# Performance work log

Measured on AMD Instinct MI355X. Metric: run time of the kernel, lower is better.

Reference implementation:

```python
import jax, jax.numpy as jnp
import numpy as np

N_NODES = 50000
N_EDGES = 800000
IN_DIM = 128
HID = 64
OUT = 64
HEADS = 4
NEG_SLOPE = 0.2  # DGL GATConv default leaky_relu negative slope


def gat_conv(x, src, dst, W, attn_l, attn_r, bias, n_heads, d_out, n_nodes):
    """DGL-style GATConv: x [N, F_in] -> [N, H, D]."""
    feat = (x @ W).reshape(n_nodes, n_heads, d_out)            # [N,H,D]
    el = jnp.sum(feat * attn_l, axis=-1)                        # [N,H]
    er = jnp.sum(feat * attn_r, axis=-1)                        # [N,H]
    e = jax.nn.leaky_relu(el[src] + er[dst], NEG_SLOPE)         # [E,H]
    # edge softmax over incoming edges of each dst node
    emax = jax.ops.segment_max(e, dst, num_segments=n_nodes)    # [N,H]
    emax = jnp.where(jnp.isfinite(emax), emax, 0.0)
    emax = jax.lax.stop_gradient(emax)
    a = jnp.exp(e - emax[dst])                                  # [E,H]
    denom = jax.ops.segment_sum(a, dst, num_segments=n_nodes)   # [N,H]
    alpha = a / jnp.maximum(denom[dst], 1e-9)                   # [E,H]
    msg = feat[src] * alpha[:, :, None]                         # [E,H,D]
    out = jax.ops.segment_sum(msg, dst, num_segments=n_nodes)   # [N,H,D]
    return out + bias.reshape(1, n_heads, d_out)


def setup_inputs() -> dict:
    key = jax.random.key(0)
    ks = jax.random.split(key, 12)
    features = jax.random.normal(ks[0], (N_NODES, IN_DIM), jnp.float32)
    src = jax.random.randint(ks[1], (N_EDGES,), 0, N_NODES)
    dst = jax.random.randint(ks[2], (N_EDGES,), 0, N_NODES)
    s1 = 1.0 / np.sqrt(IN_DIM)
    s2 = 1.0 / np.sqrt(HID * HEADS)
    return {
        "features": features,
        "src": src,
        "dst": dst,
        "W1": jax.random.normal(ks[3], (IN_DIM, HEADS * HID), jnp.float32) * s1,
        "al1": jax.random.normal(ks[4], (HEADS, HID), jnp.float32) * s1,
        "ar1": jax.random.normal(ks[5], (HEADS, HID), jnp.float32) * s1,
        "b1": jnp.zeros((HEADS * HID,), jnp.float32),
        "W2": jax.random.normal(ks[6], (HEADS * HID, HEADS * OUT), jnp.float32) * s2,
        "al2": jax.random.normal(ks[7], (HEADS, OUT), jnp.float32) * s2,
        "ar2": jax.random.normal(ks[8], (HEADS, OUT), jnp.float32) * s2,
        "b2": jnp.zeros((HEADS * OUT,), jnp.float32),
    }


def reference(features, src, dst, W1, al1, ar1, b1, W2, al2, ar2, b2):
    h = gat_conv(features, src, dst, W1, al1, ar1, b1, HEADS, HID, N_NODES)
    h = jax.nn.elu(h)                        # layer1 activation=F.elu
    h = h.reshape(N_NODES, HEADS * HID)      # .flatten(1)
    # dropout(0.2) is identity in eval mode
    h = gat_conv(h, src, dst, W2, al2, ar2, b2, HEADS, OUT, N_NODES)
    return h.mean(axis=1)                    # mean over heads -> [N, OUT]
```

## Files before the change

### kernel.cpp

```cpp
#include <hip/hip_runtime.h>
#include <hip/hip_bf16.h>
#include <math.h>

#define N_NODES 50000
#define N_EDGES 800000
#define IN_DIM 128
#define NEG_SLOPE 0.2f

typedef __attribute__((ext_vector_type(8))) short s16x8;
typedef __attribute__((ext_vector_type(4))) float f32x4;

__device__ inline unsigned short f2bf(float v) {
    unsigned u = __float_as_uint(v);
    unsigned r = (u + 0x7fffu + ((u >> 16) & 1u)) >> 16;
    return (unsigned short)r;
}
__device__ inline float bf2f(unsigned short b) {
    return __uint_as_float(((unsigned)b) << 16);
}
__device__ inline float lrelu(float v) {
    return v >= 0.f ? v : NEG_SLOPE * v;
}


__global__ void zero_int(int* __restrict__ p, int n) {
    int i = blockIdx.x * blockDim.x + threadIdx.x;
    if (i < n) p[i] = 0;
}

__global__ void hist_kernel(const int* __restrict__ dst, int* __restrict__ cnt) {
    int e = blockIdx.x * blockDim.x + threadIdx.x;
    if (e < N_EDGES) atomicAdd(&cnt[dst[e]], 1);
}

__global__ __launch_bounds__(1024) void scan_kernel(const int* __restrict__ cnt,
                                                    int* __restrict__ off, int n) {
    __shared__ int wsum[16];
    __shared__ int carry_s;
    int tid = threadIdx.x, wid = tid >> 6, lane = tid & 63;
    if (tid == 0) carry_s = 0;
    __syncthreads();
    for (int base = 0; base < n; base += 1024) {
        int i = base + tid;
        int v = (i < n) ? cnt[i] : 0;
        int x = v;
#pragma unroll
        for (int s = 1; s < 64; s <<= 1) {
            int t = __shfl_up(x, s, 64);
            if (lane >= s) x += t;
        }
        if (lane == 63) wsum[wid] = x;
        __syncthreads();
        if (wid == 0 && lane < 16) {
            int w = wsum[lane];
#pragma unroll
            for (int s = 1; s < 16; s <<= 1) {
                int t = __shfl_up(w, s, 64);
                if (lane >= s) w += t;
            }
            wsum[lane] = w;
        }
        __syncthreads();
        int woff = (wid > 0) ? wsum[wid - 1] : 0;
        int incl = carry_s + woff + x;
        if (i < n) off[i] = incl - v;
        __syncthreads();
        if (tid == 1023) carry_s = incl;
        __syncthreads();
    }
    if (threadIdx.x == 0) off[n] = carry_s;
}

__global__ void copy_int(const int* __restrict__ a, int* __restrict__ b, int n) {
    int i = blockIdx.x * blockDim.x + threadIdx.x;
    if (i < n) b[i] = a[i];
}

__global__ void scatter_kernel(const int* __restrict__ src, const int* __restrict__ dst,
                               int* __restrict__ cur, int* __restrict__ csr_src) {
    int e = blockIdx.x * blockDim.x + threadIdx.x;
    if (e < N_EDGES) {
        int d = dst[e];
        int pos = atomicAdd(&cur[d], 1);
        csr_src[pos] = src[e];
    }
}


__global__ void split_feat(const float* __restrict__ in, unsigned short* __restrict__ hi,
                           unsigned short* __restrict__ lo, int n4) {
    int i = blockIdx.x * blockDim.x + threadIdx.x;
    if (i < n4) {
        float4 v = *reinterpret_cast<const float4*>(&in[i * 4]);
        ushort4 h, l;
        h.x = f2bf(v.x); l.x = f2bf(v.x - bf2f(h.x));
        h.y = f2bf(v.y); l.y = f2bf(v.y - bf2f(h.y));
        h.z = f2bf(v.z); l.z = f2bf(v.z - bf2f(h.z));
        h.w = f2bf(v.w); l.w = f2bf(v.w - bf2f(h.w));
        *reinterpret_cast<ushort4*>(&hi[i * 4]) = h;
        *reinterpret_cast<ushort4*>(&lo[i * 4]) = l;
    }
}

template <int K>
__global__ void split_wt(const float* __restrict__ W, unsigned short* __restrict__ Bth,
                         unsigned short* __restrict__ Btl) {
    int k = blockIdx.x;
    int c = threadIdx.x;
    float v = W[(size_t)k * 256 + c];
    unsigned short h = f2bf(v);
    Bth[(size_t)c * K + k] = h;
    Btl[(size_t)c * K + k] = f2bf(v - bf2f(h));
}


#define GLDS(gsrc, loff)                                                        \
    __builtin_amdgcn_global_load_lds(                                           \
        (const __attribute__((address_space(1))) unsigned int*)(gsrc),          \
        (__attribute__((address_space(3))) unsigned int*)(lds + (loff)),        \
        16, 0, 0)

template <int K>
__global__ __launch_bounds__(256, 2) void mfma_gemm(const unsigned short* __restrict__ Ahi,
                                                    const unsigned short* __restrict__ Alo,
                                                    const unsigned short* __restrict__ Bth,
                                                    const unsigned short* __restrict__ Btl,
                                                    const float* __restrict__ attl,
                                                    const float* __restrict__ attr,
                                                    unsigned short* __restrict__ Chi,
                                                    float* __restrict__ el,
                                                    float* __restrict__ er,
                                                    int M) {
    __shared__ __align__(16) char lds[81920];
    int tid = threadIdx.x;
    int h = tid >> 6;
    int lane = tid & 63;
    int rr = lane & 15;
    int g = lane >> 4;
    int row0 = blockIdx.x * 64;

    int arow = row0 + (tid & 63);
    if (arow >= M) arow = M - 1;
    int akc = tid >> 6;
    const unsigned short* asrc_h = Ahi + (size_t)arow * K + akc * 8;
    const unsigned short* asrc_l = Alo + (size_t)arow * K + akc * 8;
    const unsigned short* bsrc_h = Bth + (size_t)tid * K;
    const unsigned short* bsrc_l = Btl + (size_t)tid * K;

    f32x4 acc[4][4] = {};

    {
        GLDS(asrc_h, tid * 16);
        GLDS(asrc_l, 4096 + tid * 16);
#pragma unroll
        for (int j = 0; j < 4; j++) {
            GLDS(bsrc_h + j * 8, 8192 + j * 4096 + tid * 16);
            GLDS(bsrc_l + j * 8, 24576 + j * 4096 + tid * 16);
        }
    }

    int cur = 0;
    for (int kb = 0; kb < K; kb += 32) {
        __syncthreads();
        if (kb + 32 < K) {
            int nb = (cur ^ 1) * 40960;
            GLDS(asrc_h + kb + 32, nb + tid * 16);
            GLDS(asrc_l + kb + 32, nb + 4096 + tid * 16);
#pragma unroll
            for (int j = 0; j < 4; j++) {
                GLDS(bsrc_h + kb + 32 + j * 8, nb + 8192 + j * 4096 + tid * 16);
                GLDS(bsrc_l + kb + 32 + j * 8, nb + 24576 + j * 4096 + tid * 16);
            }
        }
        const char* lb = lds + cur * 40960;
        s16x8 ah[4], al[4], bh[4], bl[4];
#pragma unroll
        for (int mi = 0; mi < 4; mi++) {
            int off = g * 1024 + (mi * 16 + rr) * 16;
            ah[mi] = *reinterpret_cast<const s16x8*>(lb + off);
            al[mi] = *reinterpret_cast<const s16x8*>(lb + 4096 + off);
        }
#pragma unroll
        for (int ni = 0; ni < 4; ni++) {
            int off = g * 4096 + (h * 64 + ni * 16 + rr) * 16;
            bh[ni] = *reinterpret_cast<const s16x8*>(lb + 8192 + off);
            bl[ni] = *reinterpret_cast<const s16x8*>(lb + 24576 + off);
        }
#pragma unroll
        for (int mi = 0; mi < 4; mi++) {
#pragma unroll
            for (int ni = 0; ni < 4; ni++) {
                acc[mi][ni] = __builtin_amdgcn_mfma_f32_16x16x32_bf16(ah[mi], bh[ni], acc[mi][ni], 0, 0, 0);
                acc[mi][ni] = __builtin_amdgcn_mfma_f32_16x16x32_bf16(ah[mi], bl[ni], acc[mi][ni], 0, 0, 0);
                acc[mi][ni] = __builtin_amdgcn_mfma_f32_16x16x32_bf16(al[mi], bh[ni], acc[mi][ni], 0, 0, 0);
            }
        }
        cur ^= 1;
    }

    float alv[4], arv[4];
#pragma unroll
    for (int ni = 0; ni < 4; ni++) {
        alv[ni] = attl[h * 64 + ni * 16 + rr];
        arv[ni] = attr[h * 64 + ni * 16 + rr];
    }
#pragma unroll
    for (int mi = 0; mi < 4; mi++) {
#pragma unroll
        for (int reg = 0; reg < 4; reg++) {
            int row = row0 + mi * 16 + g * 4 + reg;
            bool ok = row < M;
            float pel = 0.f, per_ = 0.f;
#pragma unroll
            for (int ni = 0; ni < 4; ni++) {
                float v = acc[mi][ni][reg];
                pel += v * alv[ni];
                per_ += v * arv[ni];
                if (ok) Chi[(size_t)row * 256 + h * 64 + ni * 16 + rr] = f2bf(v);
            }
#pragma unroll
            for (int s = 1; s < 16; s <<= 1) {
                pel  += __shfl_xor(pel, s, 64);
                per_ += __shfl_xor(per_, s, 64);
            }
            if (rr == 0 && ok) {
                el[row * 4 + h] = pel;
                er[row * 4 + h] = per_;
            }
        }
    }
}


template <int LAYER>
__global__ __launch_bounds__(256) void agg_kernel(const unsigned short* __restrict__ feat16,
                                                  const float* __restrict__ el,
                                                  const float* __restrict__ er,
                                                  const int* __restrict__ row_off,
                                                  const int* __restrict__ csr_src,
                                                  const float* __restrict__ bias,
                                                  unsigned short* __restrict__ out_hi,
                                                  unsigned short* __restrict__ out_lo,
                                                  float* __restrict__ outf) {
    int n = blockIdx.x * 4 + (threadIdx.x >> 6);
    int lane = threadIdx.x & 63;
    int h = lane >> 4;
    int js = row_off[n], je = row_off[n + 1];
    float er_nh = er[n * 4 + h];
    float m = -INFINITY, ssum = 0.f;
    float4 acc = make_float4(0.f, 0.f, 0.f, 0.f);
    int j = js;
    for (; j + 7 < je; j += 8) {
        int ss[8]; ushort4 uu[8]; float vv[8];
#pragma unroll
        for (int q = 0; q < 8; q++) ss[q] = csr_src[j + q];
#pragma unroll
        for (int q = 0; q < 8; q++)
            uu[q] = *reinterpret_cast<const ushort4*>(&feat16[(size_t)ss[q] * 256 + lane * 4]);
#pragma unroll
        for (int q = 0; q < 8; q++) vv[q] = lrelu(el[ss[q] * 4 + h] + er_nh);
        float mx = fmaxf(fmaxf(fmaxf(vv[0], vv[1]), fmaxf(vv[2], vv[3])),
                         fmaxf(fmaxf(vv[4], vv[5]), fmaxf(vv[6], vv[7])));
        float mn = fmaxf(m, mx);
        float sc = __expf(m - mn);
        float p[8];
#pragma unroll
        for (int q = 0; q < 8; q++) p[q] = __expf(vv[q] - mn);
        float psum = ((p[0] + p[1]) + (p[2] + p[3])) + ((p[4] + p[5]) + (p[6] + p[7]));
        ssum = ssum * sc + psum;
        float ax = 0.f, ay = 0.f, az = 0.f, aw = 0.f;
#pragma unroll
        for (int q = 0; q < 8; q++) {
            ax += p[q] * bf2f(uu[q].x);
            ay += p[q] * bf2f(uu[q].y);
            az += p[q] * bf2f(uu[q].z);
            aw += p[q] * bf2f(uu[q].w);
        }
        acc.x = acc.x * sc + ax;
        acc.y = acc.y * sc + ay;
        acc.z = acc.z * sc + az;
        acc.w = acc.w * sc + aw;
        m = mn;
    }
    for (; j + 3 < je; j += 4) {
        int s0 = csr_src[j], s1 = csr_src[j + 1], s2 = csr_src[j + 2], s3 = csr_src[j + 3];
        ushort4 u0 = *reinterpret_cast<const ushort4*>(&feat16[(size_t)s0 * 256 + lane * 4]);
        ushort4 u1 = *reinterpret_cast<const ushort4*>(&feat16[(size_t)s1 * 256 + lane * 4]);
        ushort4 u2 = *reinterpret_cast<const ushort4*>(&feat16[(size_t)s2 * 256 + lane * 4]);
        ushort4 u3 = *reinterpret_cast<const ushort4*>(&feat16[(size_t)s3 * 256 + lane * 4]);
        float v0 = lrelu(el[s0 * 4 + h] + er_nh);
        float v1 = lrelu(el[s1 * 4 + h] + er_nh);
        float v2 = lrelu(el[s2 * 4 + h] + er_nh);
        float v3 = lrelu(el[s3 * 4 + h] + er_nh);
        float mx = fmaxf(fmaxf(v0, v1), fmaxf(v2, v3));
        float mn = fmaxf(m, mx);
        float sc = __expf(m - mn);
        float p0 = __expf(v0 - mn);
        float p1 = __expf(v1 - mn);
        float p2 = __expf(v2 - mn);
        float p3 = __expf(v3 - mn);
        ssum = ssum * sc + ((p0 + p1) + (p2 + p3));
        acc.x = acc.x * sc + (p0 * bf2f(u0.x) + p1 * bf2f(u1.x)) + (p2 * bf2f(u2.x) + p3 * bf2f(u3.x));
        acc.y = acc.y * sc + (p0 * bf2f(u0.y) + p1 * bf2f(u1.y)) + (p2 * bf2f(u2.y) + p3 * bf2f(u3.y));
        acc.z = acc.z * sc + (p0 * bf2f(u0.z) + p1 * bf2f(u1.z)) + (p2 * bf2f(u2.z) + p3 * bf2f(u3.z));
        acc.w = acc.w * sc + (p0 * bf2f(u0.w) + p1 * bf2f(u1.w)) + (p2 * bf2f(u2.w) + p3 * bf2f(u3.w));
        m = mn;
    }
    for (; j < je; j++) {
        int s = csr_src[j];
        ushort4 u = *reinterpret_cast<const ushort4*>(&feat16[(size_t)s * 256 + lane * 4]);
        float val = lrelu(el[s * 4 + h] + er_nh);
        float mn = fmaxf(m, val);
        float sc = __expf(m - mn);
        float p = __expf(val - mn);
        ssum = ssum * sc + p;
        acc.x = acc.x * sc + p * bf2f(u.x);
        acc.y = acc.y * sc + p * bf2f(u.y);
        acc.z = acc.z * sc + p * bf2f(u.z);
        acc.w = acc.w * sc + p * bf2f(u.w);
        m = mn;
    }
    float inv = 1.f / fmaxf(ssum, 1e-9f);
    float4 res;
    res.x = acc.x * inv + bias[lane * 4 + 0];
    res.y = acc.y * inv + bias[lane * 4 + 1];
    res.z = acc.z * inv + bias[lane * 4 + 2];
    res.w = acc.w * inv + bias[lane * 4 + 3];
    if (LAYER == 1) {
        res.x = res.x > 0.f ? res.x : __expf(res.x) - 1.f;
        res.y = res.y > 0.f ? res.y : __expf(res.y) - 1.f;
        res.z = res.z > 0.f ? res.z : __expf(res.z) - 1.f;
        res.w = res.w > 0.f ? res.w : __expf(res.w) - 1.f;
        ushort4 hz, lz;
        hz.x = f2bf(res.x); lz.x = f2bf(res.x - bf2f(hz.x));
        hz.y = f2bf(res.y); lz.y = f2bf(res.y - bf2f(hz.y));
        hz.z = f2bf(res.z); lz.z = f2bf(res.z - bf2f(hz.z));
        hz.w = f2bf(res.w); lz.w = f2bf(res.w - bf2f(hz.w));
        *reinterpret_cast<ushort4*>(&out_hi[(size_t)n * 256 + lane * 4]) = hz;
        *reinterpret_cast<ushort4*>(&out_lo[(size_t)n * 256 + lane * 4]) = lz;
    } else {
#pragma unroll
        for (int mask = 16; mask <= 32; mask <<= 1) {
            res.x += __shfl_xor(res.x, mask, 64);
            res.y += __shfl_xor(res.y, mask, 64);
            res.z += __shfl_xor(res.z, mask, 64);
            res.w += __shfl_xor(res.w, mask, 64);
        }
        if (lane < 16) {
            float4 o = make_float4(res.x * 0.25f, res.y * 0.25f, res.z * 0.25f, res.w * 0.25f);
            *reinterpret_cast<float4*>(&outf[(size_t)n * 64 + lane * 4]) = o;
        }
    }
}


extern "C" void kernel_launch(void* const* d_in, const int* in_sizes, int n_in,
                              void* d_out, int out_size, void* d_ws, size_t ws_size,
                              hipStream_t stream) {
    const float* features = (const float*)d_in[0];
    const int*   src      = (const int*)d_in[1];
    const int*   dst      = (const int*)d_in[2];
    const float* W1       = (const float*)d_in[3];
    const float* al1      = (const float*)d_in[4];
    const float* ar1      = (const float*)d_in[5];
    const float* b1       = (const float*)d_in[6];
    const float* W2       = (const float*)d_in[7];
    const float* al2      = (const float*)d_in[8];
    const float* ar2      = (const float*)d_in[9];
    const float* b2       = (const float*)d_in[10];
    float* out = (float*)d_out;

    char* ws = (char*)d_ws;
    unsigned short* feat16  = (unsigned short*)(ws);
    unsigned short* h1_hi   = (unsigned short*)(ws + 25600000);
    unsigned short* h1_lo   = (unsigned short*)(ws + 51200000);
    unsigned short* fA_hi   = (unsigned short*)(ws + 76800000);
    unsigned short* fA_lo   = (unsigned short*)(ws + 89600000);
    unsigned short* Bt1_hi  = (unsigned short*)(ws + 102400000);
    unsigned short* Bt1_lo  = (unsigned short*)(ws + 102465536);
    unsigned short* Bt2_hi  = (unsigned short*)(ws + 102531072);
    unsigned short* Bt2_lo  = (unsigned short*)(ws + 102662144);
    float*          el      = (float*)(ws + 102793216);
    float*          er      = (float*)(ws + 103593216);
    int*            row_off = (int*)  (ws + 104393216);
    int*            cur     = (int*)  (ws + 104593280);
    int*            csr     = (int*)  (ws + 104793280);

    zero_int<<<(N_NODES + 255) / 256, 256, 0, stream>>>(cur, N_NODES);
    hist_kernel<<<(N_EDGES + 255) / 256, 256, 0, stream>>>(dst, cur);
    scan_kernel<<<1, 1024, 0, stream>>>(cur, row_off, N_NODES);
    copy_int<<<(N_NODES + 255) / 256, 256, 0, stream>>>(row_off, cur, N_NODES);
    scatter_kernel<<<(N_EDGES + 255) / 256, 256, 0, stream>>>(src, dst, cur, csr);

    split_feat<<<(N_NODES * IN_DIM / 4 + 255) / 256, 256, 0, stream>>>(
        features, fA_hi, fA_lo, N_NODES * IN_DIM / 4);
    split_wt<IN_DIM><<<IN_DIM, 256, 0, stream>>>(W1, Bt1_hi, Bt1_lo);
    split_wt<256><<<256, 256, 0, stream>>>(W2, Bt2_hi, Bt2_lo);

    int gemm_blocks = (N_NODES + 63) / 64;

    mfma_gemm<IN_DIM><<<gemm_blocks, 256, 0, stream>>>(
        fA_hi, fA_lo, Bt1_hi, Bt1_lo, al1, ar1, feat16, el, er, N_NODES);
    agg_kernel<1><<<12500, 256, 0, stream>>>(feat16, el, er, row_off, csr, b1, h1_hi, h1_lo, nullptr);

    mfma_gemm<256><<<gemm_blocks, 256, 0, stream>>>(
        h1_hi, h1_lo, Bt2_hi, Bt2_lo, al2, ar2, feat16, el, er, N_NODES);
    agg_kernel<2><<<12500, 256, 0, stream>>>(feat16, el, er, row_off, csr, b2, nullptr, nullptr, out);
}
```

Baseline: 401.0 us.

## Fold attention vectors into weights and compute el/er via extra MFMA column

Precomputes W·attn_l and W·attn_r per head as split-bf16 vectors, so el/er come out of extra MFMA accumulations during the GEMM instead of a shuffle-reduction epilogue. The GEMM tile grows to 128 rows with 512 threads so each B tile loaded into LDS is reused across twice as many rows. B rows are permuted so each lane writes four contiguous bf16 outputs with one vector store. The trade-offs are a larger LDS footprint, lower occupancy, and different rounding in el/er, which now come from bf16-split products instead of fp32 accumulation.

```diff
diff --git a/kernel.cpp b/kernel.cpp
--- a/kernel.cpp
+++ b/kernel.cpp
@@ -107,10 +107,35 @@
                          unsigned short* __restrict__ Btl) {
     int k = blockIdx.x;
     int c = threadIdx.x;
+    int h = c >> 6, w = c & 63;
+    int row = h * 64 + (w & 3) * 16 + (w >> 2);
     float v = W[(size_t)k * 256 + c];
-    unsigned short h = f2bf(v);
-    Bth[(size_t)c * K + k] = h;
-    Btl[(size_t)c * K + k] = f2bf(v - bf2f(h));
+    unsigned short hh = f2bf(v);
+    Bth[(size_t)row * K + k] = hh;
+    Btl[(size_t)row * K + k] = f2bf(v - bf2f(hh));
+}
+
+template <int K>
+__global__ void wlr_kernel(const float* __restrict__ W, const float* __restrict__ al,
+                           const float* __restrict__ ar,
+                           unsigned short* __restrict__ EhC, unsigned short* __restrict__ ElC) {
+    int k = blockIdx.x * blockDim.x + threadIdx.x;
+    if (k >= K) return;
+#pragma unroll
+    for (int h = 0; h < 4; h++) {
+        float sl = 0.f, sr = 0.f;
+        for (int c = 0; c < 64; c++) {
+            float w = W[(size_t)k * 256 + h * 64 + c];
+            sl += w * al[h * 64 + c];
+            sr += w * ar[h * 64 + c];
+        }
+        unsigned short hh = f2bf(sl);
+        EhC[(size_t)(h * 2 + 0) * K + k] = hh;
+        ElC[(size_t)(h * 2 + 0) * K + k] = f2bf(sl - bf2f(hh));
+        hh = f2bf(sr);
+        EhC[(size_t)(h * 2 + 1) * K + k] = hh;
+        ElC[(size_t)(h * 2 + 1) * K + k] = f2bf(sr - bf2f(hh));
+    }
 }
 
 
@@ -121,70 +146,79 @@
         16, 0, 0)
 
 template <int K>
-__global__ __launch_bounds__(256, 2) void mfma_gemm(const unsigned short* __restrict__ Ahi,
-                                                    const unsigned short* __restrict__ Alo,
-                                                    const unsigned short* __restrict__ Bth,
-                                                    const unsigned short* __restrict__ Btl,
-                                                    const float* __restrict__ attl,
-                                                    const float* __restrict__ attr,
-                                                    unsigned short* __restrict__ Chi,
-                                                    float* __restrict__ el,
-                                                    float* __restrict__ er,
-                                                    int M) {
-    __shared__ __align__(16) char lds[81920];
+__global__ __launch_bounds__(512) void mfma_gemm(const unsigned short* __restrict__ Ahi,
+                                                 const unsigned short* __restrict__ Alo,
+                                                 const unsigned short* __restrict__ Bth,
+                                                 const unsigned short* __restrict__ Btl,
+                                                 const unsigned short* __restrict__ EhC,
+                                                 const unsigned short* __restrict__ ElC,
+                                                 unsigned short* __restrict__ Chi,
+                                                 float* __restrict__ el,
+                                                 float* __restrict__ er,
+                                                 int M) {
+    __shared__ __align__(16) char lds[98304];
     int tid = threadIdx.x;
-    int h = tid >> 6;
+    int w = tid >> 6;
+    int h = w & 3;
+    int r2 = w >> 2;
     int lane = tid & 63;
     int rr = lane & 15;
     int g = lane >> 4;
-    int row0 = blockIdx.x * 64;
-
-    int arow = row0 + (tid & 63);
+    int row0 = blockIdx.x * 128;
+
+    int arow = row0 + (tid & 127);
     if (arow >= M) arow = M - 1;
-    int akc = tid >> 6;
+    int akc = (tid >> 7) & 3;
     const unsigned short* asrc_h = Ahi + (size_t)arow * K + akc * 8;
     const unsigned short* asrc_l = Alo + (size_t)arow * K + akc * 8;
-    const unsigned short* bsrc_h = Bth + (size_t)tid * K;
-    const unsigned short* bsrc_l = Btl + (size_t)tid * K;
+    int btrow = tid & 255;
+    int bkc = (tid >> 8) * 2;
+    const unsigned short* bsrc_h = Bth + (size_t)btrow * K + bkc * 8;
+    const unsigned short* bsrc_l = Btl + (size_t)btrow * K + bkc * 8;
+    int bdst0 = 16384 + bkc * 4096 + btrow * 16;
+    int bdst1 = 16384 + (bkc + 1) * 4096 + btrow * 16;
 
     f32x4 acc[4][4] = {};
-
-    {
-        GLDS(asrc_h, tid * 16);
-        GLDS(asrc_l, 4096 + tid * 16);
-#pragma unroll
-        for (int j = 0; j < 4; j++) {
-            GLDS(bsrc_h + j * 8, 8192 + j * 4096 + tid * 16);
-            GLDS(bsrc_l + j * 8, 24576 + j * 4096 + tid * 16);
-        }
-    }
+    f32x4 acce[4] = {};
+
+    GLDS(asrc_h, tid * 16);
+    GLDS(asrc_l, 8192 + tid * 16);
+    GLDS(bsrc_h, bdst0);
+    GLDS(bsrc_h + 8, bdst1);
+    GLDS(bsrc_l, 16384 + bdst0);
+    GLDS(bsrc_l + 8, 16384 + bdst1);
 
     int cur = 0;
     for (int kb = 0; kb < K; kb += 32) {
         __syncthreads();
         if (kb + 32 < K) {
-            int nb = (cur ^ 1) * 40960;
+            int nb = (cur ^ 1) * 49152;
             GLDS(asrc_h + kb + 32, nb + tid * 16);
-            GLDS(asrc_l + kb + 32, nb + 4096 + tid * 16);
-#pragma unroll
-            for (int j = 0; j < 4; j++) {
-                GLDS(bsrc_h + kb + 32 + j * 8, nb + 8192 + j * 4096 + tid * 16);
-                GLDS(bsrc_l + kb + 32 + j * 8, nb + 24576 + j * 4096 + tid * 16);
-            }
-        }
-        const char* lb = lds + cur * 40960;
+            GLDS(asrc_l + kb + 32, nb + 8192 + tid * 16);
+            GLDS(bsrc_h + kb + 32, nb + bdst0);
+            GLDS(bsrc_h + kb + 40, nb + bdst1);
+            GLDS(bsrc_l + kb + 32, nb + 16384 + bdst0);
+            GLDS(bsrc_l + kb + 40, nb + 16384 + bdst1);
+        }
+        s16x8 ehf = {};
+        s16x8 elf = {};
+        if (rr < 2) {
+            ehf = *reinterpret_cast<const s16x8*>(EhC + (size_t)(h * 2 + rr) * K + kb + g * 8);
+            elf = *reinterpret_cast<const s16x8*>(ElC + (size_t)(h * 2 + rr) * K + kb + g * 8);
+        }
+        const char* lb = lds + cur * 49152;
         s16x8 ah[4], al[4], bh[4], bl[4];
 #pragma unroll
         for (int mi = 0; mi < 4; mi++) {
-            int off = g * 1024 + (mi * 16 + rr) * 16;
+            int off = g * 2048 + (r2 * 64 + mi * 16 + rr) * 16;
             ah[mi] = *reinterpret_cast<const s16x8*>(lb + off);
-            al[mi] = *reinterpret_cast<const s16x8*>(lb + 4096 + off);
+            al[mi] = *reinterpret_cast<const s16x8*>(lb + 8192 + off);
         }
 #pragma unroll
         for (int ni = 0; ni < 4; ni++) {
             int off = g * 4096 + (h * 64 + ni * 16 + rr) * 16;
-            bh[ni] = *reinterpret_cast<const s16x8*>(lb + 8192 + off);
-            bl[ni] = *reinterpret_cast<const s16x8*>(lb + 24576 + off);
+            bh[ni] = *reinterpret_cast<const s16x8*>(lb + 16384 + off);
+            bl[ni] = *reinterpret_cast<const s16x8*>(lb + 32768 + off);
         }
 #pragma unroll
         for (int mi = 0; mi < 4; mi++) {
@@ -194,38 +228,27 @@
                 acc[mi][ni] = __builtin_amdgcn_mfma_f32_16x16x32_bf16(ah[mi], bl[ni], acc[mi][ni], 0, 0, 0);
                 acc[mi][ni] = __builtin_amdgcn_mfma_f32_16x16x32_bf16(al[mi], bh[ni], acc[mi][ni], 0, 0, 0);
             }
+            acce[mi] = __builtin_amdgcn_mfma_f32_16x16x32_bf16(ah[mi], ehf, acce[mi], 0, 0, 0);
+            acce[mi] = __builtin_amdgcn_mfma_f32_16x16x32_bf16(ah[mi], elf, acce[mi], 0, 0, 0);
+            acce[mi] = __builtin_amdgcn_mfma_f32_16x16x32_bf16(al[mi], ehf, acce[mi], 0, 0, 0);
         }
         cur ^= 1;
     }
 
-    float alv[4], arv[4];
-#pragma unroll
-    for (int ni = 0; ni < 4; ni++) {
-        alv[ni] = attl[h * 64 + ni * 16 + rr];
-        arv[ni] = attr[h * 64 + ni * 16 + rr];
-    }
 #pragma unroll
     for (int mi = 0; mi < 4; mi++) {
 #pragma unroll
         for (int reg = 0; reg < 4; reg++) {
-            int row = row0 + mi * 16 + g * 4 + reg;
-            bool ok = row < M;
-            float pel = 0.f, per_ = 0.f;
-#pragma unroll
-            for (int ni = 0; ni < 4; ni++) {
-                float v = acc[mi][ni][reg];
-                pel += v * alv[ni];
-                per_ += v * arv[ni];
-                if (ok) Chi[(size_t)row * 256 + h * 64 + ni * 16 + rr] = f2bf(v);
-            }
-#pragma unroll
-            for (int s = 1; s < 16; s <<= 1) {
-                pel  += __shfl_xor(pel, s, 64);
-                per_ += __shfl_xor(per_, s, 64);
-            }
-            if (rr == 0 && ok) {
-                el[row * 4 + h] = pel;
-                er[row * 4 + h] = per_;
+            int row = row0 + r2 * 64 + mi * 16 + g * 4 + reg;
+            if (row < M) {
+                ushort4 u;
+                u.x = f2bf(acc[mi][0][reg]);
+                u.y = f2bf(acc[mi][1][reg]);
+                u.z = f2bf(acc[mi][2][reg]);
+                u.w = f2bf(acc[mi][3][reg]);
+                *reinterpret_cast<ushort4*>(&Chi[(size_t)row * 256 + h * 64 + rr * 4]) = u;
+                if (rr == 0) el[row * 4 + h] = acce[mi][reg];
+                if (rr == 1) er[row * 4 + h] = acce[mi][reg];
             }
         }
     }
@@ -380,11 +403,15 @@
     unsigned short* Bt1_lo  = (unsigned short*)(ws + 102465536);
     unsigned short* Bt2_hi  = (unsigned short*)(ws + 102531072);
     unsigned short* Bt2_lo  = (unsigned short*)(ws + 102662144);
-    float*          el      = (float*)(ws + 102793216);
-    float*          er      = (float*)(ws + 103593216);
-    int*            row_off = (int*)  (ws + 104393216);
-    int*            cur     = (int*)  (ws + 104593280);
-    int*            csr     = (int*)  (ws + 104793280);
+    unsigned short* E1C_hi  = (unsigned short*)(ws + 102793216);
+    unsigned short* E1C_lo  = (unsigned short*)(ws + 102795264);
+    unsigned short* E2C_hi  = (unsigned short*)(ws + 102797312);
+    unsigned short* E2C_lo  = (unsigned short*)(ws + 102801408);
+    float*          el      = (float*)(ws + 102805504);
+    float*          er      = (float*)(ws + 103605504);
+    int*            row_off = (int*)  (ws + 104405504);
+    int*            cur     = (int*)  (ws + 104605568);
+    int*            csr     = (int*)  (ws + 104805568);
 
     zero_int<<<(N_NODES + 255) / 256, 256, 0, stream>>>(cur, N_NODES);
     hist_kernel<<<(N_EDGES + 255) / 256, 256, 0, stream>>>(dst, cur);
@@ -396,14 +423,16 @@
         features, fA_hi, fA_lo, N_NODES * IN_DIM / 4);
     split_wt<IN_DIM><<<IN_DIM, 256, 0, stream>>>(W1, Bt1_hi, Bt1_lo);
     split_wt<256><<<256, 256, 0, stream>>>(W2, Bt2_hi, Bt2_lo);
-
-    int gemm_blocks = (N_NODES + 63) / 64;
-
-    mfma_gemm<IN_DIM><<<gemm_blocks, 256, 0, stream>>>(
-        fA_hi, fA_lo, Bt1_hi, Bt1_lo, al1, ar1, feat16, el, er, N_NODES);
+    wlr_kernel<IN_DIM><<<1, IN_DIM, 0, stream>>>(W1, al1, ar1, E1C_hi, E1C_lo);
+    wlr_kernel<256><<<1, 256, 0, stream>>>(W2, al2, ar2, E2C_hi, E2C_lo);
+
+    int gemm_blocks = (N_NODES + 127) / 128;
+
+    mfma_gemm<IN_DIM><<<gemm_blocks, 512, 0, stream>>>(
+        fA_hi, fA_lo, Bt1_hi, Bt1_lo, E1C_hi, E1C_lo, feat16, el, er, N_NODES);
     agg_kernel<1><<<12500, 256, 0, stream>>>(feat16, el, er, row_off, csr, b1, h1_hi, h1_lo, nullptr);
 
-    mfma_gemm<256><<<gemm_blocks, 256, 0, stream>>>(
-        h1_hi, h1_lo, Bt2_hi, Bt2_lo, al2, ar2, feat16, el, er, N_NODES);
+    mfma_gemm<256><<<gemm_blocks, 512, 0, stream>>>(
+        h1_hi, h1_lo, Bt2_hi, Bt2_lo, E2C_hi, E2C_lo, feat16, el, er, N_NODES);
     agg_kernel<2><<<12500, 256, 0, stream>>>(feat16, el, er, row_off, csr, b2, nullptr, nullptr, out);
 }
```

New measurement: 391.0 us. 2.5% less time.
